# Optimization experiments

Hardware: AMD Instinct MI355X
Metric: run time of the kernel (lower is better)

The kernel has to match this reference:

```python
import jax, jax.numpy as jnp
import numpy as np

B, S, E, H = 16, 512, 1024, 16
DK = E // H  # 64


def setup_inputs() -> dict:
    key = jax.random.key(0)
    ks = jax.random.split(key, 14)
    s_e = 1.0 / np.sqrt(E)
    s_d = 1.0 / np.sqrt(DK)
    return {
        "inp": jax.random.normal(ks[0], (B, S, E), dtype=jnp.float32),
        # projection linears (torch Linear stored as x @ W + b with W pre-transposed)
        "Wq": jax.random.uniform(ks[1], (E, E), jnp.float32, -s_e, s_e),
        "bq": jax.random.uniform(ks[2], (E,), jnp.float32, -s_e, s_e),
        "Wk": jax.random.uniform(ks[3], (E, E), jnp.float32, -s_e, s_e),
        "bk": jax.random.uniform(ks[4], (E,), jnp.float32, -s_e, s_e),
        "Wv": jax.random.uniform(ks[5], (E, E), jnp.float32, -s_e, s_e),
        "bv": jax.random.uniform(ks[6], (E,), jnp.float32, -s_e, s_e),
        # per-head gating linears
        "Wfq": jax.random.uniform(ks[7], (DK, DK), jnp.float32, -s_d, s_d),
        "bfq": jax.random.uniform(ks[8], (DK,), jnp.float32, -s_d, s_d),
        "Wfk": jax.random.uniform(ks[9], (DK, DK), jnp.float32, -s_d, s_d),
        "bfk": jax.random.uniform(ks[10], (DK,), jnp.float32, -s_d, s_d),
        "Wfg": jax.random.uniform(ks[11], (DK, 2 * DK), jnp.float32, -s_d, s_d),
        "bfg": jax.random.uniform(ks[12], (2 * DK,), jnp.float32, -s_d, s_d),
    }


def _split_heads(x):
    # [B, S, E] -> [B, H, S, DK]
    b, s, _ = x.shape
    return x.reshape(b, s, H, DK).transpose(0, 2, 1, 3)


def reference(inp, Wq, bq, Wk, bk, Wv, bv, Wfq, bfq, Wfk, bfk, Wfg, bfg):
    q = _split_heads(inp @ Wq + bq)  # [B,H,S,DK]
    k = _split_heads(inp @ Wk + bk)
    v = _split_heads(inp @ Wv + bv)

    # gated query/key modulation
    G = (q @ Wfq + bfq) * (k @ Wfk + bfk)          # [B,H,S,DK]
    M = jax.nn.sigmoid(G @ Wfg + bfg)              # [B,H,S,2*DK]
    q = q * M[..., :DK]
    k = k * M[..., DK:]

    scores = jnp.einsum("bhqd,bhkd->bhqk", q, k) / jnp.sqrt(jnp.asarray(DK, q.dtype))
    p_attn = jax.nn.softmax(scores, axis=-1)
    x = jnp.einsum("bhqk,bhkd->bhqd", p_attn, v)   # [B,H,S,DK]
    return x.transpose(0, 2, 1, 3).reshape(inp.shape[0], -1, H * DK)
```

## Files before the change

kernel.cpp:

```cpp
#include <hip/hip_runtime.h>


typedef __bf16 bf16;
typedef __bf16 bf16x8 __attribute__((ext_vector_type(8)));
typedef __bf16 bf16x4 __attribute__((ext_vector_type(4)));
typedef float  f32x4  __attribute__((ext_vector_type(4)));

#define MFMA16(a,b,c) __builtin_amdgcn_mfma_f32_16x16x32_bf16((a),(b),(c),0,0,0)

#define GLL16(gp, lp)                                                          \
  __builtin_amdgcn_global_load_lds(                                            \
      (__attribute__((address_space(1))) void*)(void*)(gp),                    \
      (__attribute__((address_space(3))) void*)(lp), 16, 0, 0)

__global__ __launch_bounds__(256) void k_prep(const float* __restrict__ in,
                                              bf16* __restrict__ Xb,
                                              const float* __restrict__ Wq,
                                              const float* __restrict__ Wk,
                                              const float* __restrict__ Wv,
                                              bf16* __restrict__ WT) {
  __shared__ float tile[32][33];
  const int bx = blockIdx.x, t = threadIdx.x;
  if (bx < 8192) {
    int i = bx * 256 + t;
    float4 v = ((const float4*)in)[i];
    bf16x4 o;
    o[0] = (bf16)v.x; o[1] = (bf16)v.y; o[2] = (bf16)v.z; o[3] = (bf16)v.w;
    ((bf16x4*)Xb)[i] = o;
  } else {
    int r = bx - 8192;
    int mat = r >> 10; r &= 1023;
    int kb = r >> 5, nb = r & 31;
    const float* W = (mat == 0) ? Wq : ((mat == 1) ? Wk : Wv);
    bf16* O = WT + (size_t)mat * (1024 * 1024);
    const int tr = t >> 3, tc = (t & 7) * 4;
    float4 v = *(const float4*)&W[(size_t)(kb * 32 + tr) * 1024 + nb * 32 + tc];
    tile[tr][tc] = v.x; tile[tr][tc + 1] = v.y;
    tile[tr][tc + 2] = v.z; tile[tr][tc + 3] = v.w;
    __syncthreads();
    bf16x4 o;
    o[0] = (bf16)tile[tc][tr];     o[1] = (bf16)tile[tc + 1][tr];
    o[2] = (bf16)tile[tc + 2][tr]; o[3] = (bf16)tile[tc + 3][tr];
    *(bf16x4*)&O[(size_t)(nb * 32 + tr) * 1024 + kb * 32 + tc] = o;
  }
}

__global__ __launch_bounds__(256, 2) void k_proj(const bf16* __restrict__ X,
                                                 const bf16* __restrict__ WT,
                                                 const float* __restrict__ bq,
                                                 const float* __restrict__ bk,
                                                 const float* __restrict__ bv,
                                                 bf16* __restrict__ qw,
                                                 bf16* __restrict__ kw,
                                                 bf16* __restrict__ vt) {
  extern __shared__ bf16 lds[];
  bf16* As = lds;
  bf16* Bs = lds + 16384;

  const int tid = threadIdx.x;
  const int m0 = blockIdx.x * 128;
  const int n0 = blockIdx.y * 192;

  const int l = tid & 63, wid = tid >> 6;
  const int wm = wid >> 1, wn = wid & 1;
  const int l4 = l & 15, q8 = l >> 4;
  const int cs0 = (q8 ^ (l4 & 7)) * 8;
  const int arow = (wm * 64 + l4) * 64;
  const int brow = (wn * 96 + l4) * 64;

  const int srow = tid >> 3;
  const int scol = ((tid & 7) ^ (srow & 7)) * 8;
  const bf16* Xs = X + (size_t)(m0 + srow) * 1024 + scol;
  const bf16* Ws = WT + (size_t)(n0 + srow) * 1024 + scol;
  const int ldst = tid * 8;

#define STG_AU(bf, kt, u)                                                      \
  GLL16(Xs + (size_t)(u) * 32768 + (kt) * 64,                                  \
        As + (bf) * 8192 + (u) * 2048 + ldst)
#define STG_BU(bf, kt, u)                                                      \
  GLL16(Ws + (size_t)(u) * 32768 + (kt) * 64,                                  \
        Bs + (bf) * 12288 + (u) * 2048 + ldst)

  f32x4 acc[4][6] = {};
  bf16x8 aa[2], bb0[6], bb1[6];

#define LDA2(bf, qm, kk)                                                       \
  do {                                                                         \
    _Pragma("unroll") for (int m_ = 0; m_ < 2; ++m_)                           \
        aa[m_] = *(const bf16x8*)&As[(bf) * 8192 + arow + (qm) * 2048 +        \
                                     m_ * 1024 + (cs0 ^ ((kk) * 32))];         \
  } while (0)
#define LDB6(bf, kk, arr)                                                      \
  do {                                                                         \
    _Pragma("unroll") for (int n_ = 0; n_ < 6; ++n_)                           \
        arr[n_] = *(const bf16x8*)&Bs[(bf) * 12288 + brow + n_ * 1024 +        \
                                      (cs0 ^ ((kk) * 32))];                    \
  } while (0)
#define MMQ(qm, arr)                                                           \
  do {                                                                         \
    _Pragma("unroll") for (int m_ = 0; m_ < 2; ++m_)                           \
    _Pragma("unroll") for (int n_ = 0; n_ < 6; ++n_)                           \
        acc[(qm) * 2 + m_][n_] =                                               \
            MFMA16(arr[n_], aa[m_], acc[(qm) * 2 + m_][n_]);                   \
  } while (0)
#define PH_PRE                                                                 \
  __builtin_amdgcn_s_barrier();                                                \
  asm volatile("s_waitcnt lgkmcnt(0)" ::: "memory");                           \
  __builtin_amdgcn_s_setprio(1)
#define PH_POST                                                                \
  __builtin_amdgcn_s_setprio(0);                                               \
  __builtin_amdgcn_s_barrier()

  STG_AU(0, 0, 0); STG_AU(0, 0, 1); STG_AU(0, 0, 2); STG_AU(0, 0, 3);
  STG_BU(0, 0, 0); STG_BU(0, 0, 1); STG_BU(0, 0, 2);
  STG_BU(0, 0, 3); STG_BU(0, 0, 4); STG_BU(0, 0, 5);
  STG_BU(1, 1, 0); STG_BU(1, 1, 1); STG_BU(1, 1, 2);
  STG_BU(1, 1, 3); STG_BU(1, 1, 4); STG_BU(1, 1, 5);
  asm volatile("s_waitcnt vmcnt(6)" ::: "memory");
  __builtin_amdgcn_s_barrier();

#pragma unroll 1
  for (int i = 0; i < 8; ++i) {
    const int t1 = 2 * i + 1;
    const int t2 = (i < 7) ? 2 * i + 2 : 14;
    const int t3 = (i < 7) ? 2 * i + 3 : 15;
    LDB6(0, 0, bb0); LDA2(0, 0, 0);
    STG_AU(1, t1, 0); STG_AU(1, t1, 1);
    PH_PRE; MMQ(0, bb0); PH_POST;
    LDB6(0, 1, bb1); LDA2(0, 1, 0);
    STG_AU(1, t1, 2); STG_AU(1, t1, 3);
    PH_PRE; MMQ(1, bb0); PH_POST;
    LDA2(0, 0, 1);
    STG_BU(0, t2, 0); STG_BU(0, t2, 1); STG_BU(0, t2, 2);
    PH_PRE; MMQ(0, bb1); PH_POST;
    LDA2(0, 1, 1);
    STG_BU(0, t2, 3); STG_BU(0, t2, 4); STG_BU(0, t2, 5);
    PH_PRE; MMQ(1, bb1);
    __builtin_amdgcn_s_setprio(0);
    asm volatile("s_waitcnt vmcnt(6)" ::: "memory");
    __builtin_amdgcn_s_barrier();
    LDB6(1, 0, bb0); LDA2(1, 0, 0);
    STG_AU(0, t2, 0); STG_AU(0, t2, 1);
    PH_PRE; MMQ(0, bb0); PH_POST;
    LDB6(1, 1, bb1); LDA2(1, 1, 0);
    STG_AU(0, t2, 2); STG_AU(0, t2, 3);
    PH_PRE; MMQ(1, bb0); PH_POST;
    LDA2(1, 0, 1);
    STG_BU(1, t3, 0); STG_BU(1, t3, 1); STG_BU(1, t3, 2);
    PH_PRE; MMQ(0, bb1); PH_POST;
    LDA2(1, 1, 1);
    STG_BU(1, t3, 3); STG_BU(1, t3, 4); STG_BU(1, t3, 5);
    PH_PRE; MMQ(1, bb1);
    __builtin_amdgcn_s_setprio(0);
    asm volatile("s_waitcnt vmcnt(6)" ::: "memory");
    __builtin_amdgcn_s_barrier();
  }

#pragma unroll
  for (int mi = 0; mi < 4; ++mi) {
    const int m = m0 + wm * 64 + mi * 16 + l4;
    const int b_ = m >> 9, s = m & 511;
#pragma unroll
    for (int nj = 0; nj < 6; ++nj) {
      const int n = n0 + wn * 96 + nj * 16 + q8 * 4;
      const int mat = n >> 10, nn = n & 1023;
      if (mat == 2) {
        const int h = nn >> 6, d0 = nn & 63;
#pragma unroll
        for (int r = 0; r < 4; ++r) {
          vt[((size_t)(b_ * 16 + h) * 64 + d0 + r) * 512 + s] =
              (bf16)(acc[mi][nj][r] + bv[nn + r]);
        }
      } else {
        const float* bias = (mat == 0) ? bq : bk;
        const float4 bb = *(const float4*)&bias[nn];
        bf16x4 o;
        o[0] = (bf16)(acc[mi][nj][0] + bb.x);
        o[1] = (bf16)(acc[mi][nj][1] + bb.y);
        o[2] = (bf16)(acc[mi][nj][2] + bb.z);
        o[3] = (bf16)(acc[mi][nj][3] + bb.w);
        bf16* dst = (mat == 0) ? qw : kw;
        *(bf16x4*)&dst[(size_t)m * 1024 + nn] = o;
      }
    }
  }
#undef STG_AU
#undef STG_BU
#undef LDA2
#undef LDB6
#undef MMQ
#undef PH_PRE
#undef PH_POST
}

__global__ __launch_bounds__(256, 2) void k_gate(bf16* __restrict__ qw,
                                                 bf16* __restrict__ kw,
                                                 const float* __restrict__ Wfq,
                                                 const float* __restrict__ bfq,
                                                 const float* __restrict__ Wfk,
                                                 const float* __restrict__ bfk,
                                                 const float* __restrict__ Wfg,
                                                 const float* __restrict__ bfg) {
  __shared__ __align__(16) char smraw[56320];
  bf16* sWq = (bf16*)smraw;
  bf16* sWk = (bf16*)(smraw + 9216);
  bf16* sWg = (bf16*)(smraw + 18432);
  bf16* sG  = (bf16*)(smraw + 36864);
  float* sb = (float*)(smraw + 55296);
  bf16* Ms  = (bf16*)smraw;
  const int tid = threadIdx.x;

  for (int idx = tid; idx < 4096; idx += 256) {
    int k = idx >> 6, n = idx & 63;
    sWq[n * 72 + k] = (bf16)Wfq[k * 64 + n];
    sWk[n * 72 + k] = (bf16)Wfk[k * 64 + n];
  }
  for (int idx = tid; idx < 8192; idx += 256) {
    int k = idx >> 7, n = idx & 127;
    sWg[n * 72 + k] = (bf16)Wfg[k * 128 + n];
  }
  if (tid < 64) { sb[tid] = bfq[tid]; sb[64 + tid] = bfk[tid]; }
  if (tid < 128) sb[128 + tid] = bfg[tid];
  __syncthreads();

  const int w = tid >> 6, l = tid & 63, l4 = l & 15, q8 = l >> 4;
  const int T0 = blockIdx.x * 128;
  const int rbase = w * 32;

  bf16x8 aq[2][2], ak[2][2];
#pragma unroll
  for (int i = 0; i < 2; ++i)
#pragma unroll
    for (int kk = 0; kk < 2; ++kk) {
      size_t off = (size_t)(T0 + rbase + i * 16 + l4) * 64 + kk * 32 + q8 * 8;
      aq[i][kk] = *(const bf16x8*)&qw[off];
      ak[i][kk] = *(const bf16x8*)&kw[off];
    }

  f32x4 fqc[2][4] = {}, fkc[2][4] = {};
#pragma unroll
  for (int j = 0; j < 4; ++j) {
    bf16x8 bq0 = *(const bf16x8*)&sWq[(j * 16 + l4) * 72 + q8 * 8];
    bf16x8 bq1 = *(const bf16x8*)&sWq[(j * 16 + l4) * 72 + 32 + q8 * 8];
    bf16x8 bk0 = *(const bf16x8*)&sWk[(j * 16 + l4) * 72 + q8 * 8];
    bf16x8 bk1 = *(const bf16x8*)&sWk[(j * 16 + l4) * 72 + 32 + q8 * 8];
#pragma unroll
    for (int i = 0; i < 2; ++i) {
      fqc[i][j] = MFMA16(aq[i][0], bq0, fqc[i][j]);
      fqc[i][j] = MFMA16(aq[i][1], bq1, fqc[i][j]);
      fkc[i][j] = MFMA16(ak[i][0], bk0, fkc[i][j]);
      fkc[i][j] = MFMA16(ak[i][1], bk1, fkc[i][j]);
    }
  }

#pragma unroll
  for (int j = 0; j < 4; ++j) {
    float bqb = sb[j * 16 + l4], bkb = sb[64 + j * 16 + l4];
#pragma unroll
    for (int i = 0; i < 2; ++i)
#pragma unroll
      for (int r = 0; r < 4; ++r) {
        int row = rbase + i * 16 + q8 * 4 + r;
        float g = (fqc[i][j][r] + bqb) * (fkc[i][j][r] + bkb);
        sG[row * 72 + j * 16 + l4] = (bf16)g;
      }
  }
  __syncthreads();

  bf16x8 ag[2][2];
#pragma unroll
  for (int i = 0; i < 2; ++i)
#pragma unroll
    for (int kk = 0; kk < 2; ++kk)
      ag[i][kk] = *(const bf16x8*)&sG[(rbase + i * 16 + l4) * 72 + kk * 32 + q8 * 8];
  f32x4 mc[2][8] = {};
#pragma unroll
  for (int jj = 0; jj < 8; ++jj) {
    bf16x8 bg0 = *(const bf16x8*)&sWg[(jj * 16 + l4) * 72 + q8 * 8];
    bf16x8 bg1 = *(const bf16x8*)&sWg[(jj * 16 + l4) * 72 + 32 + q8 * 8];
#pragma unroll
    for (int i = 0; i < 2; ++i) {
      mc[i][jj] = MFMA16(ag[i][0], bg0, mc[i][jj]);
      mc[i][jj] = MFMA16(ag[i][1], bg1, mc[i][jj]);
    }
  }

  __syncthreads();
#pragma unroll
  for (int jj = 0; jj < 8; ++jj) {
    float bgb = sb[128 + jj * 16 + l4];
#pragma unroll
    for (int i = 0; i < 2; ++i)
#pragma unroll
      for (int r = 0; r < 4; ++r) {
        int row = rbase + i * 16 + q8 * 4 + r;
        float m = mc[i][jj][r] + bgb;
        Ms[row * 136 + jj * 16 + l4] = (bf16)(1.0f / (1.0f + __expf(-m)));
      }
  }
  __syncthreads();

  const float SC = 0.18033688011112042f;
  const int tl = tid >> 1, half = tid & 1;
  bf16* base = (half ? kw : qw) + (size_t)(T0 + tl) * 64;
  const float scl = half ? 1.0f : SC;
#pragma unroll
  for (int c = 0; c < 8; ++c) {
    bf16x8 v = *(const bf16x8*)&base[c * 8];
    bf16x8 m = *(const bf16x8*)&Ms[tl * 136 + half * 64 + c * 8];
    bf16x8 o;
#pragma unroll
    for (int e = 0; e < 8; ++e)
      o[e] = (bf16)((float)v[e] * (float)m[e] * scl);
    *(bf16x8*)&base[c * 8] = o;
  }
}

__global__ __launch_bounds__(256, 2) void k_attn(const bf16* __restrict__ qw,
                                                 const bf16* __restrict__ kw,
                                                 const bf16* __restrict__ vt,
                                                 float* __restrict__ out) {
  __shared__ bf16 Kt[128 * 72];
  __shared__ bf16 Vt[64 * 136];
  __shared__ bf16 Pb[4][32 * 40];
  const int tid = threadIdx.x, w = tid >> 6, l = tid & 63;
  const int l4 = l & 15, q8 = l >> 4;
  const int bx = blockIdx.x;
  const int slot = bx >> 3;
  const int qc = slot & 3;
  const int bh = (bx & 7) + 8 * (slot >> 2);
  const int b_ = bh >> 4, h = bh & 15;
  bf16* Pw = &Pb[w][0];

  bf16x8 qf[2][2];
#pragma unroll
  for (int i = 0; i < 2; ++i)
#pragma unroll
    for (int kk = 0; kk < 2; ++kk) {
      int s = qc * 128 + w * 32 + i * 16 + l4;
      qf[i][kk] = *(const bf16x8*)
          &qw[(((size_t)b_ * 512 + s) * 16 + h) * 64 + kk * 32 + q8 * 8];
    }

  f32x4 o[2][4] = {};
  float mrun[2][4], lrun[2][4];
#pragma unroll
  for (int i = 0; i < 2; ++i)
#pragma unroll
    for (int r = 0; r < 4; ++r) { mrun[i][r] = -3.0e38f; lrun[i][r] = 0.0f; }

  for (int t = 0; t < 4; ++t) {
    __syncthreads();
#pragma unroll
    for (int i = 0; i < 4; ++i) {
      int chunk = i * 256 + tid;
      {
        int key = chunk >> 3, c8 = chunk & 7;
        bf16x8 v = *(const bf16x8*)
            &kw[(((size_t)b_ * 512 + t * 128 + key) * 16 + h) * 64 + c8 * 8];
        *(bf16x8*)&Kt[key * 72 + c8 * 8] = v;
      }
      {
        int d = chunk >> 4, c16 = chunk & 15;
        bf16x8 v = *(const bf16x8*)
            &vt[((size_t)bh * 64 + d) * 512 + t * 128 + c16 * 8];
        *(bf16x8*)&Vt[d * 136 + c16 * 8] = v;
      }
    }
    __syncthreads();

    f32x4 sc[2][8];
    const f32x4 fz = {};
#pragma unroll
    for (int c = 0; c < 8; ++c) {
      bf16x8 kb0 = *(const bf16x8*)&Kt[(c * 16 + l4) * 72 + q8 * 8];
      sc[0][c] = MFMA16(qf[0][0], kb0, fz);
      sc[1][c] = MFMA16(qf[1][0], kb0, fz);
      bf16x8 kb1 = *(const bf16x8*)&Kt[(c * 16 + l4) * 72 + 32 + q8 * 8];
      sc[0][c] = MFMA16(qf[0][1], kb1, sc[0][c]);
      sc[1][c] = MFMA16(qf[1][1], kb1, sc[1][c]);
    }

#pragma unroll
    for (int i = 0; i < 2; ++i) {
      float al[4];
#pragma unroll
      for (int r = 0; r < 4; ++r) {
        float mx = sc[i][0][r];
#pragma unroll
        for (int c = 1; c < 8; ++c) mx = fmaxf(mx, sc[i][c][r]);
        mx = fmaxf(mx, __shfl_xor(mx, 1));
        mx = fmaxf(mx, __shfl_xor(mx, 2));
        mx = fmaxf(mx, __shfl_xor(mx, 4));
        mx = fmaxf(mx, __shfl_xor(mx, 8));
        float mn = fmaxf(mrun[i][r], mx);
        al[r] = exp2f(mrun[i][r] - mn);
        mrun[i][r] = mn;
        float sm = 0.0f;
#pragma unroll
        for (int c = 0; c < 8; ++c) {
          float p = exp2f(sc[i][c][r] - mn);
          sc[i][c][r] = p;
          sm += p;
        }
        sm += __shfl_xor(sm, 1); sm += __shfl_xor(sm, 2);
        sm += __shfl_xor(sm, 4); sm += __shfl_xor(sm, 8);
        lrun[i][r] = lrun[i][r] * al[r] + sm;
      }
#pragma unroll
      for (int f = 0; f < 4; ++f)
#pragma unroll
        for (int r = 0; r < 4; ++r) o[i][f][r] *= al[r];
    }

#pragma unroll
    for (int kk2 = 0; kk2 < 4; ++kk2) {
#pragma unroll
      for (int i = 0; i < 2; ++i)
#pragma unroll
        for (int cc = 0; cc < 2; ++cc) {
          int c = kk2 * 2 + cc;
#pragma unroll
          for (int r = 0; r < 4; ++r)
            Pw[(i * 16 + q8 * 4 + r) * 40 + cc * 16 + l4] = (bf16)sc[i][c][r];
        }
      bf16x8 pa0 = *(const bf16x8*)&Pw[(l4) * 40 + q8 * 8];
      bf16x8 pa1 = *(const bf16x8*)&Pw[(16 + l4) * 40 + q8 * 8];
#pragma unroll
      for (int f = 0; f < 4; ++f) {
        bf16x8 vb = *(const bf16x8*)&Vt[(f * 16 + l4) * 136 + kk2 * 32 + q8 * 8];
        o[0][f] = MFMA16(pa0, vb, o[0][f]);
        o[1][f] = MFMA16(pa1, vb, o[1][f]);
      }
    }
  }

#pragma unroll
  for (int i = 0; i < 2; ++i)
#pragma unroll
    for (int r = 0; r < 4; ++r) {
      int srow = qc * 128 + w * 32 + i * 16 + q8 * 4 + r;
      float inv = 1.0f / lrun[i][r];
#pragma unroll
      for (int f = 0; f < 4; ++f)
        out[(((size_t)b_ * 512 + srow) * 16 + h) * 64 + f * 16 + l4] =
            o[i][f][r] * inv;
    }
}

extern "C" void kernel_launch(void* const* d_in, const int* in_sizes, int n_in,
                              void* d_out, int out_size, void* d_ws,
                              size_t ws_size, hipStream_t stream) {
  (void)in_sizes; (void)n_in; (void)out_size; (void)ws_size;
  const float* inp = (const float*)d_in[0];
  const float* Wq  = (const float*)d_in[1];
  const float* bq  = (const float*)d_in[2];
  const float* Wk  = (const float*)d_in[3];
  const float* bk  = (const float*)d_in[4];
  const float* Wv  = (const float*)d_in[5];
  const float* bv  = (const float*)d_in[6];
  const float* Wfq = (const float*)d_in[7];
  const float* bfq = (const float*)d_in[8];
  const float* Wfk = (const float*)d_in[9];
  const float* bfk = (const float*)d_in[10];
  const float* Wfg = (const float*)d_in[11];
  const float* bfg = (const float*)d_in[12];
  float* out = (float*)d_out;

  static bool s_attr = false;
  if (!s_attr) {
    (void)hipFuncSetAttribute((const void*)k_proj,
                              hipFuncAttributeMaxDynamicSharedMemorySize,
                              81920);
    s_attr = true;
  }

  char* ws = (char*)d_ws;
  bf16* Xb = (bf16*)(ws);
  bf16* WT = (bf16*)(ws + 16777216);
  bf16* qw = (bf16*)(ws + 16777216 + 6291456);
  bf16* kw = qw + 8388608;
  bf16* vt = kw + 8388608;

  k_prep<<<11264, 256, 0, stream>>>(inp, Xb, Wq, Wk, Wv, WT);
  k_proj<<<dim3(64, 16), 256, 81920, stream>>>(Xb, WT, bq, bk, bv, qw, kw, vt);
  k_gate<<<1024, 256, 0, stream>>>(qw, kw, Wfq, bfq, Wfk, bfk, Wfg, bfg);
  k_attn<<<1024, 256, 0, stream>>>(qw, kw, vt, out);
}
```

Baseline: 246.2 us.

## Alias P scratch onto K tile, raise occupancy, lazy softmax rescale, MFMA priority

Drops the separate P staging buffer and reuses the K tile's LDS once the QK^T MFMAs finish, with an added barrier so every wave is done reading K first. This cuts LDS per block, and the launch bound goes from 2 to 4 blocks per SM to raise occupancy. The online softmax now rescales O and l only when some row max grows by more than 8 in log2 units, skipping most rescale multiplies at the cost of bounded exponent growth. s_setprio is raised around the MFMA blocks to favour issuing matrix ops. The extra barrier and a tighter register budget could cost time.

```diff
diff --git a/kernel.cpp b/kernel.cpp
--- a/kernel.cpp
+++ b/kernel.cpp
@@ -316,13 +316,12 @@
   }
 }
 
-__global__ __launch_bounds__(256, 2) void k_attn(const bf16* __restrict__ qw,
+__global__ __launch_bounds__(256, 4) void k_attn(const bf16* __restrict__ qw,
                                                  const bf16* __restrict__ kw,
                                                  const bf16* __restrict__ vt,
                                                  float* __restrict__ out) {
   __shared__ bf16 Kt[128 * 72];
   __shared__ bf16 Vt[64 * 136];
-  __shared__ bf16 Pb[4][32 * 40];
   const int tid = threadIdx.x, w = tid >> 6, l = tid & 63;
   const int l4 = l & 15, q8 = l >> 4;
   const int bx = blockIdx.x;
@@ -330,7 +329,7 @@
   const int qc = slot & 3;
   const int bh = (bx & 7) + 8 * (slot >> 2);
   const int b_ = bh >> 4, h = bh & 15;
-  bf16* Pw = &Pb[w][0];
+  bf16* Pw = Kt + w * 1280;
 
   bf16x8 qf[2][2];
 #pragma unroll
@@ -371,6 +370,7 @@
 
     f32x4 sc[2][8];
     const f32x4 fz = {};
+    __builtin_amdgcn_s_setprio(1);
 #pragma unroll
     for (int c = 0; c < 8; ++c) {
       bf16x8 kb0 = *(const bf16x8*)&Kt[(c * 16 + l4) * 72 + q8 * 8];
@@ -380,37 +380,53 @@
       sc[0][c] = MFMA16(qf[0][1], kb1, sc[0][c]);
       sc[1][c] = MFMA16(qf[1][1], kb1, sc[1][c]);
     }
+    __builtin_amdgcn_s_setprio(0);
+    __syncthreads();
 
 #pragma unroll
     for (int i = 0; i < 2; ++i) {
-      float al[4];
+      float mx[4];
 #pragma unroll
       for (int r = 0; r < 4; ++r) {
-        float mx = sc[i][0][r];
-#pragma unroll
-        for (int c = 1; c < 8; ++c) mx = fmaxf(mx, sc[i][c][r]);
-        mx = fmaxf(mx, __shfl_xor(mx, 1));
-        mx = fmaxf(mx, __shfl_xor(mx, 2));
-        mx = fmaxf(mx, __shfl_xor(mx, 4));
-        mx = fmaxf(mx, __shfl_xor(mx, 8));
-        float mn = fmaxf(mrun[i][r], mx);
-        al[r] = exp2f(mrun[i][r] - mn);
-        mrun[i][r] = mn;
+        float m2 = sc[i][0][r];
+#pragma unroll
+        for (int c = 1; c < 8; ++c) m2 = fmaxf(m2, sc[i][c][r]);
+        m2 = fmaxf(m2, __shfl_xor(m2, 1));
+        m2 = fmaxf(m2, __shfl_xor(m2, 2));
+        m2 = fmaxf(m2, __shfl_xor(m2, 4));
+        m2 = fmaxf(m2, __shfl_xor(m2, 8));
+        mx[r] = m2;
+      }
+      bool grow = false;
+#pragma unroll
+      for (int r = 0; r < 4; ++r) grow = grow || (mx[r] > mrun[i][r] + 8.0f);
+      if (__any(grow)) {
+        float al[4];
+#pragma unroll
+        for (int r = 0; r < 4; ++r) {
+          float mn = fmaxf(mrun[i][r], mx[r]);
+          al[r] = exp2f(mrun[i][r] - mn);
+          mrun[i][r] = mn;
+          lrun[i][r] *= al[r];
+        }
+#pragma unroll
+        for (int f = 0; f < 4; ++f)
+#pragma unroll
+          for (int r = 0; r < 4; ++r) o[i][f][r] *= al[r];
+      }
+#pragma unroll
+      for (int r = 0; r < 4; ++r) {
         float sm = 0.0f;
 #pragma unroll
         for (int c = 0; c < 8; ++c) {
-          float p = exp2f(sc[i][c][r] - mn);
+          float p = exp2f(sc[i][c][r] - mrun[i][r]);
           sc[i][c][r] = p;
           sm += p;
         }
         sm += __shfl_xor(sm, 1); sm += __shfl_xor(sm, 2);
         sm += __shfl_xor(sm, 4); sm += __shfl_xor(sm, 8);
-        lrun[i][r] = lrun[i][r] * al[r] + sm;
-      }
-#pragma unroll
-      for (int f = 0; f < 4; ++f)
-#pragma unroll
-        for (int r = 0; r < 4; ++r) o[i][f][r] *= al[r];
+        lrun[i][r] += sm;
+      }
     }
 
 #pragma unroll
@@ -426,12 +442,14 @@
         }
       bf16x8 pa0 = *(const bf16x8*)&Pw[(l4) * 40 + q8 * 8];
       bf16x8 pa1 = *(const bf16x8*)&Pw[(16 + l4) * 40 + q8 * 8];
+      __builtin_amdgcn_s_setprio(1);
 #pragma unroll
       for (int f = 0; f < 4; ++f) {
         bf16x8 vb = *(const bf16x8*)&Vt[(f * 16 + l4) * 136 + kk2 * 32 + q8 * 8];
         o[0][f] = MFMA16(pa0, vb, o[0][f]);
         o[1][f] = MFMA16(pa1, vb, o[1][f]);
       }
+      __builtin_amdgcn_s_setprio(0);
     }
   }
 
```

Result: slower. 302.6 us (+22.9%).
